# Optimization experiments

Measured on AMD Instinct MI355X. Metric: run time of the kernel, lower is better.

The kernel has to match this reference:

```python
import jax, jax.numpy as jnp
import numpy as np
import math

B, L, D, H = 2, 2048, 1024, 16
DK = D // H  # 64


def _lin(k, din, dout):
    kw, kb = jax.random.split(k)
    w = jax.random.normal(kw, (din, dout), dtype=jnp.float32) * 0.02
    b = jax.random.normal(kb, (dout,), dtype=jnp.float32) * 0.02
    return w, b


def setup_inputs() -> dict:
    key = jax.random.key(0)
    ks = jax.random.split(key, 12)
    wq, bq = _lin(ks[0], D, D)
    wk, bk = _lin(ks[1], D, D)
    wv, bv = _lin(ks[2], D, D)
    wo, bo = _lin(ks[3], D, D)
    whq, bhq = _lin(ks[4], DK, DK)
    whk, bhk = _lin(ks[5], DK, DK)
    whv, bhv = _lin(ks[6], DK, DK)
    who, bho = _lin(ks[7], DK, DK)
    return {
        "q_input": jax.random.normal(ks[8], (B, L, D), dtype=jnp.float32),
        "k_input": jax.random.normal(ks[9], (B, L, D), dtype=jnp.float32),
        "v_input": jax.random.normal(ks[10], (B, L, D), dtype=jnp.float32),
        "mask": jnp.ones((B, 1, L, L), dtype=jnp.int32),
        "wq": wq, "bq": bq, "wk": wk, "bk": bk, "wv": wv, "bv": bv,
        "wo": wo, "bo": bo,
        "whq": whq, "bhq": bhq, "whk": whk, "bhk": bhk,
        "whv": whv, "bhv": bhv, "who": who, "bho": bho,
    }


def reference(q_input, k_input, v_input, mask, wq, bq, wk, bk, wv, bv, wo, bo,
              whq, bhq, whk, bhk, whv, bhv, who, bho):
    scale = 1.0 / math.sqrt(DK)
    # Q/K/V projections -> [B, H, L, DK]
    Q = (q_input @ wq + bq).reshape(B, L, H, DK).transpose(0, 2, 1, 3)
    K = (k_input @ wk + bk).reshape(B, L, H, DK).transpose(0, 2, 1, 3)
    V = (v_input @ wv + bv).reshape(B, L, H, DK).transpose(0, 2, 1, 3)
    scores = jnp.einsum('bhqd,bhkd->bhqk', Q, K) * scale  # [B,H,L,L]
    neg = jnp.finfo(scores.dtype).min
    scores = jnp.where(mask == 0, neg, scores)
    probs = jax.nn.softmax(scores, axis=-1)  # dropout is identity in eval
    attn = jnp.einsum('bhqk,bhkd->bhqd', probs, V)
    heads = attn.transpose(0, 2, 1, 3)  # [B, L, H, DK]
    # Inter-head attention over the head dimension (size H) per position
    Qh = heads @ whq + bhq
    Kh = heads @ whk + bhk
    Vh = heads @ whv + bhv
    inter = jnp.einsum('blhd,blgd->blhg', Qh, Kh) * scale  # [B,L,H,H]
    iprobs = jax.nn.softmax(inter, axis=-1)
    mixed = jnp.einsum('blhg,blgd->blhd', iprobs, Vh)  # [B,L,H,DK]
    # note: inter_head_out is defined but unused in the original forward
    concat = mixed.reshape(B, L, D)
    return concat @ wo + bo
```

## Files before the change

kernel.cpp:

```cpp
#include <hip/hip_runtime.h>
#include <hip/hip_bf16.h>

typedef __bf16 bf16_t;
typedef __bf16 bf16x8 __attribute__((ext_vector_type(8)));
typedef float f32x4 __attribute__((ext_vector_type(4)));

__global__ void transpose_qkvw_kernel(const float* __restrict__ wq, const float* __restrict__ wk,
                                      const float* __restrict__ wv, bf16_t* __restrict__ wqkvT)
{
    __shared__ bf16_t tile[64][65];
    int z = blockIdx.z;
    const float* src = (z == 0) ? wq : (z == 1) ? wk : wv;
    bf16_t* dst = wqkvT + (size_t)z * 1048576;
    int rB = blockIdx.y * 64, cB = blockIdx.x * 64;
    int t = threadIdx.x;
#pragma unroll
    for (int i = 0; i < 16; i++) {
        int e = t + i * 256; int r = e >> 6, c = e & 63;
        tile[r][c] = (bf16_t)src[(size_t)(rB + r) * 1024 + cB + c];
    }
    __syncthreads();
#pragma unroll
    for (int i = 0; i < 16; i++) {
        int e = t + i * 256; int r = e >> 6, c = e & 63;
        dst[(size_t)(cB + r) * 1024 + rB + c] = tile[c][r];
    }
}

__global__ void transpose_one_kernel(const float* __restrict__ src, bf16_t* __restrict__ dst)
{
    __shared__ bf16_t tile[64][65];
    int rB = blockIdx.y * 64, cB = blockIdx.x * 64;
    int t = threadIdx.x;
#pragma unroll
    for (int i = 0; i < 16; i++) {
        int e = t + i * 256; int r = e >> 6, c = e & 63;
        tile[r][c] = (bf16_t)src[(size_t)(rB + r) * 1024 + cB + c];
    }
    __syncthreads();
#pragma unroll
    for (int i = 0; i < 16; i++) {
        int e = t + i * 256; int r = e >> 6, c = e & 63;
        dst[(size_t)(cB + r) * 1024 + rB + c] = tile[c][r];
    }
}

__global__ void transpose_small_kernel(const float* __restrict__ s0, const float* __restrict__ s1,
                                       const float* __restrict__ s2,
                                       bf16_t* __restrict__ d0, bf16_t* __restrict__ d1, bf16_t* __restrict__ d2)
{
    int z = blockIdx.x;
    const float* src = (z == 0) ? s0 : (z == 1) ? s1 : s2;
    bf16_t* dst = (z == 0) ? d0 : (z == 1) ? d1 : d2;
    int t = threadIdx.x;
#pragma unroll
    for (int i = 0; i < 16; i++) {
        int e = t + i * 256; int r = e >> 6, c = e & 63;
        dst[c * 64 + r] = (bf16_t)src[r * 64 + c];
    }
}

__global__ void maskflags_kernel(const int* __restrict__ mask, int* __restrict__ flags)
{
    int tile = blockIdx.x;
    int b = tile >> 10, qt = (tile >> 5) & 31, kt = tile & 31;
    int ok = 1;
#pragma unroll
    for (int i = 0; i < 16; i++) {
        int e = threadIdx.x + i * 256; int r = e >> 6, c = e & 63;
        ok &= (mask[((size_t)b * 2048 + qt * 64 + r) * 2048 + kt * 64 + c] != 0) ? 1 : 0;
    }
    ok = __syncthreads_and(ok);
    if (threadIdx.x == 0) flags[tile] = ok;
}

#define GS 40

__global__ __launch_bounds__(256, 2) void gemm_qkv_kernel(
    const float* __restrict__ Aq, const float* __restrict__ Ak, const float* __restrict__ Av,
    const bf16_t* __restrict__ WT,
    const float* __restrict__ bq, const float* __restrict__ bk, const float* __restrict__ bv,
    bf16_t* __restrict__ outbase)
{
    __shared__ bf16_t As[128 * GS];
    __shared__ bf16_t Bs[128 * GS];
    const int z = blockIdx.z;
    const float* A    = (z == 0) ? Aq : (z == 1) ? Ak : Av;
    const bf16_t* Bt  = WT + (size_t)z * 1048576;
    const float* bia  = (z == 0) ? bq : (z == 1) ? bk : bv;
    bf16_t* out = outbase + (size_t)z * 4194304;

    const int t = threadIdx.x;
    const int w = t >> 6, lane = t & 63;
    const int lane15 = lane & 15, quad = lane >> 4;
    const int wr = w >> 1, wc = w & 1;
    const int rowBase = blockIdx.y * 128, colBase = blockIdx.x * 128;

    const int ar = t >> 1, ac = (t & 1) * 16;
    const int e0 = t * 8, e1 = (256 + t) * 8;
    const int r0 = e0 >> 5, c0 = e0 & 31;
    const int r1 = e1 >> 5, c1 = e1 & 31;

    f32x4 acc[4][4];
    f32x4 zf = {0.f, 0.f, 0.f, 0.f};
#pragma unroll
    for (int i = 0; i < 4; i++)
#pragma unroll
        for (int j = 0; j < 4; j++) acc[i][j] = zf;

    for (int k0 = 0; k0 < 1024; k0 += 32) {
        const float4* ap = (const float4*)(A + (size_t)(rowBase + ar) * 1024 + k0 + ac);
        float4 af4[4];
#pragma unroll
        for (int i = 0; i < 4; i++) af4[i] = ap[i];
        bf16x8 b0 = *(const bf16x8*)(Bt + (size_t)(colBase + r0) * 1024 + k0 + c0);
        bf16x8 b1 = *(const bf16x8*)(Bt + (size_t)(colBase + r1) * 1024 + k0 + c1);
        bf16x8 av0, av1;
#pragma unroll
        for (int i = 0; i < 4; i++) {
            bf16x8& dstv = (i < 2) ? av0 : av1;
            int base = (i & 1) * 4;
            dstv[base + 0] = (bf16_t)af4[i].x; dstv[base + 1] = (bf16_t)af4[i].y;
            dstv[base + 2] = (bf16_t)af4[i].z; dstv[base + 3] = (bf16_t)af4[i].w;
        }
        *(bf16x8*)(As + ar * GS + ac) = av0;
        *(bf16x8*)(As + ar * GS + ac + 8) = av1;
        *(bf16x8*)(Bs + r0 * GS + c0) = b0;
        *(bf16x8*)(Bs + r1 * GS + c1) = b1;
        __syncthreads();
        bf16x8 afr[4], bfr[4];
#pragma unroll
        for (int mi = 0; mi < 4; mi++)
            afr[mi] = *(const bf16x8*)(As + (wr * 64 + mi * 16 + lane15) * GS + quad * 8);
#pragma unroll
        for (int ni = 0; ni < 4; ni++)
            bfr[ni] = *(const bf16x8*)(Bs + (wc * 64 + ni * 16 + lane15) * GS + quad * 8);
#pragma unroll
        for (int mi = 0; mi < 4; mi++)
#pragma unroll
            for (int ni = 0; ni < 4; ni++)
                acc[mi][ni] = __builtin_amdgcn_mfma_f32_16x16x32_bf16(afr[mi], bfr[ni], acc[mi][ni], 0, 0, 0);
        __syncthreads();
    }

#pragma unroll
    for (int ni = 0; ni < 4; ni++) {
        int col = colBase + wc * 64 + ni * 16 + lane15;
        float bias = bia[col];
        int h = col >> 6, dk = col & 63;
#pragma unroll
        for (int mi = 0; mi < 4; mi++) {
#pragma unroll
            for (int r = 0; r < 4; r++) {
                int row = rowBase + wr * 64 + mi * 16 + quad * 4 + r;
                int b = row >> 11, l = row & 2047;
                float v = acc[mi][ni][r] + bias;
                size_t dst = (z < 2) ? ((((size_t)(b * 16 + h)) * 2048 + l) * 64 + dk)
                                     : ((((size_t)(b * 16 + h)) * 64 + dk) * 2048 + l);
                out[dst] = (bf16_t)v;
            }
        }
    }
}

__global__ __launch_bounds__(256, 2) void gemm_out_kernel(
    const bf16_t* __restrict__ A, const bf16_t* __restrict__ Bt,
    const float* __restrict__ bia, float* __restrict__ out)
{
    __shared__ bf16_t As[128 * GS];
    __shared__ bf16_t Bs[128 * GS];
    const int t = threadIdx.x;
    const int w = t >> 6, lane = t & 63;
    const int lane15 = lane & 15, quad = lane >> 4;
    const int wr = w >> 1, wc = w & 1;
    const int rowBase = blockIdx.y * 128, colBase = blockIdx.x * 128;
    const int e0 = t * 8, e1 = (256 + t) * 8;
    const int r0 = e0 >> 5, c0 = e0 & 31;
    const int r1 = e1 >> 5, c1 = e1 & 31;

    f32x4 acc[4][4];
    f32x4 zf = {0.f, 0.f, 0.f, 0.f};
#pragma unroll
    for (int i = 0; i < 4; i++)
#pragma unroll
        for (int j = 0; j < 4; j++) acc[i][j] = zf;

    for (int k0 = 0; k0 < 1024; k0 += 32) {
        bf16x8 a0 = *(const bf16x8*)(A  + (size_t)(rowBase + r0) * 1024 + k0 + c0);
        bf16x8 a1 = *(const bf16x8*)(A  + (size_t)(rowBase + r1) * 1024 + k0 + c1);
        bf16x8 b0 = *(const bf16x8*)(Bt + (size_t)(colBase + r0) * 1024 + k0 + c0);
        bf16x8 b1 = *(const bf16x8*)(Bt + (size_t)(colBase + r1) * 1024 + k0 + c1);
        *(bf16x8*)(As + r0 * GS + c0) = a0;
        *(bf16x8*)(As + r1 * GS + c1) = a1;
        *(bf16x8*)(Bs + r0 * GS + c0) = b0;
        *(bf16x8*)(Bs + r1 * GS + c1) = b1;
        __syncthreads();
        bf16x8 afr[4], bfr[4];
#pragma unroll
        for (int mi = 0; mi < 4; mi++)
            afr[mi] = *(const bf16x8*)(As + (wr * 64 + mi * 16 + lane15) * GS + quad * 8);
#pragma unroll
        for (int ni = 0; ni < 4; ni++)
            bfr[ni] = *(const bf16x8*)(Bs + (wc * 64 + ni * 16 + lane15) * GS + quad * 8);
#pragma unroll
        for (int mi = 0; mi < 4; mi++)
#pragma unroll
            for (int ni = 0; ni < 4; ni++)
                acc[mi][ni] = __builtin_amdgcn_mfma_f32_16x16x32_bf16(afr[mi], bfr[ni], acc[mi][ni], 0, 0, 0);
        __syncthreads();
    }

#pragma unroll
    for (int ni = 0; ni < 4; ni++) {
        int col = colBase + wc * 64 + ni * 16 + lane15;
        float bias = bia[col];
#pragma unroll
        for (int mi = 0; mi < 4; mi++) {
#pragma unroll
            for (int r = 0; r < 4; r++) {
                int row = rowBase + wr * 64 + mi * 16 + quad * 4 + r;
                out[(size_t)row * 1024 + col] = acc[mi][ni][r] + bias;
            }
        }
    }
}

#define FS 72

__global__ __launch_bounds__(256, 2) void flash_kernel(
    const bf16_t* __restrict__ QKV, const int* __restrict__ mask,
    const int* __restrict__ flags, bf16_t* __restrict__ attnout)
{
    __shared__ bf16_t Ks[2][64 * FS];
    __shared__ bf16_t Vs[2][64 * FS];
    __shared__ bf16_t Ps[4 * 16 * FS];
    const int t = threadIdx.x, w = t >> 6, lane = t & 63;
    const int lane15 = lane & 15, quad = lane >> 4;
    const int qt = blockIdx.x, bh = blockIdx.y;
    const int b = bh >> 4, h = bh & 15;
    const bf16_t* Q  = QKV;
    const bf16_t* K  = QKV + 4194304;
    const bf16_t* Vt = QKV + 8388608;
    const int qrow0 = qt * 64 + w * 16;

    const bf16_t* qb = Q + ((size_t)bh * 2048 + qrow0 + lane15) * 64;
    bf16x8 aq0 = *(const bf16x8*)(qb + quad * 8);
    bf16x8 aq1 = *(const bf16x8*)(qb + 32 + quad * 8);
#pragma unroll
    for (int j = 0; j < 8; j++) {
        aq0[j] = (bf16_t)((float)aq0[j] * 0.125f);
        aq1[j] = (bf16_t)((float)aq1[j] * 0.125f);
    }

    f32x4 o[4];
    f32x4 zf = {0.f, 0.f, 0.f, 0.f};
#pragma unroll
    for (int df = 0; df < 4; df++) o[df] = zf;
    f32x4 lsum = zf;
    bf16_t* Pw = Ps + w * 16 * FS;
    bf16x8 ones;
#pragma unroll
    for (int j = 0; j < 8; j++) ones[j] = (bf16_t)1.0f;

    const int e0 = t * 8, e1 = (256 + t) * 8;
    const int kr0 = e0 >> 6, kc0 = e0 & 63, kr1 = e1 >> 6, kc1 = e1 & 63;
    const int* flagrow = flags + (b * 32 + qt) * 32;
    const bf16_t* Kb  = K  + (size_t)bh * 2048 * 64;
    const bf16_t* Vtb = Vt + (size_t)bh * 64 * 2048;

    {
        bf16x8 k0v = *(const bf16x8*)(Kb  + (size_t)kr0 * 64 + kc0);
        bf16x8 k1v = *(const bf16x8*)(Kb  + (size_t)kr1 * 64 + kc1);
        bf16x8 v0v = *(const bf16x8*)(Vtb + (size_t)kr0 * 2048 + kc0);
        bf16x8 v1v = *(const bf16x8*)(Vtb + (size_t)kr1 * 2048 + kc1);
        *(bf16x8*)(Ks[0] + kr0 * FS + kc0) = k0v;
        *(bf16x8*)(Ks[0] + kr1 * FS + kc1) = k1v;
        *(bf16x8*)(Vs[0] + kr0 * FS + kc0) = v0v;
        *(bf16x8*)(Vs[0] + kr1 * FS + kc1) = v1v;
    }
    __syncthreads();

    for (int kt = 0; kt < 32; kt++) {
        const int cur = kt & 1, nxt = cur ^ 1;
        bf16x8 k0v, k1v, v0v, v1v;
        if (kt + 1 < 32) {
            int kn = (kt + 1) * 64;
            k0v = *(const bf16x8*)(Kb  + (size_t)(kn + kr0) * 64 + kc0);
            k1v = *(const bf16x8*)(Kb  + (size_t)(kn + kr1) * 64 + kc1);
            v0v = *(const bf16x8*)(Vtb + (size_t)kr0 * 2048 + kn + kc0);
            v1v = *(const bf16x8*)(Vtb + (size_t)kr1 * 2048 + kn + kc1);
        }

        f32x4 sf[4];
#pragma unroll
        for (int nf = 0; nf < 4; nf++) {
            f32x4 a = zf;
            bf16x8 kb0 = *(const bf16x8*)(Ks[cur] + (nf * 16 + lane15) * FS + quad * 8);
            bf16x8 kb1 = *(const bf16x8*)(Ks[cur] + (nf * 16 + lane15) * FS + 32 + quad * 8);
            a = __builtin_amdgcn_mfma_f32_16x16x32_bf16(aq0, kb0, a, 0, 0, 0);
            a = __builtin_amdgcn_mfma_f32_16x16x32_bf16(aq1, kb1, a, 0, 0, 0);
            sf[nf] = a * 1.44269504f;
        }
        if (kt + 1 < 32) {
            *(bf16x8*)(Ks[nxt] + kr0 * FS + kc0) = k0v;
            *(bf16x8*)(Ks[nxt] + kr1 * FS + kc1) = k1v;
            *(bf16x8*)(Vs[nxt] + kr0 * FS + kc0) = v0v;
            *(bf16x8*)(Vs[nxt] + kr1 * FS + kc1) = v1v;
        }
        if (!flagrow[kt]) {
#pragma unroll
            for (int nf = 0; nf < 4; nf++)
#pragma unroll
                for (int r = 0; r < 4; r++) {
                    int qrow = qrow0 + quad * 4 + r;
                    int kpos = kt * 64 + nf * 16 + lane15;
                    if (mask[((size_t)b * 2048 + qrow) * 2048 + kpos] == 0)
                        sf[nf][r] = -1e30f;
                }
        }
#pragma unroll
        for (int nf = 0; nf < 4; nf++)
#pragma unroll
            for (int r = 0; r < 4; r++)
                Pw[(quad * 4 + r) * FS + nf * 16 + lane15] =
                    (bf16_t)exp2f(fminf(sf[nf][r], 80.f));

        bf16x8 pa0 = *(const bf16x8*)(Pw + lane15 * FS + quad * 8);
        bf16x8 pa1 = *(const bf16x8*)(Pw + lane15 * FS + 32 + quad * 8);
        lsum = __builtin_amdgcn_mfma_f32_16x16x32_bf16(pa0, ones, lsum, 0, 0, 0);
        lsum = __builtin_amdgcn_mfma_f32_16x16x32_bf16(pa1, ones, lsum, 0, 0, 0);
#pragma unroll
        for (int df = 0; df < 4; df++) {
            bf16x8 vb0 = *(const bf16x8*)(Vs[cur] + (df * 16 + lane15) * FS + quad * 8);
            bf16x8 vb1 = *(const bf16x8*)(Vs[cur] + (df * 16 + lane15) * FS + 32 + quad * 8);
            o[df] = __builtin_amdgcn_mfma_f32_16x16x32_bf16(pa0, vb0, o[df], 0, 0, 0);
            o[df] = __builtin_amdgcn_mfma_f32_16x16x32_bf16(pa1, vb1, o[df], 0, 0, 0);
        }
        __syncthreads();
    }
#pragma unroll
    for (int r = 0; r < 4; r++) {
        float inv = 1.0f / lsum[r];
        size_t row = (size_t)b * 2048 + qrow0 + quad * 4 + r;
#pragma unroll
        for (int df = 0; df < 4; df++)
            attnout[(row * 16 + h) * 64 + df * 16 + lane15] = (bf16_t)(o[df][r] * inv);
    }
}

__global__ __launch_bounds__(256, 2) void interhead_kernel(
    const bf16_t* __restrict__ attn,
    const bf16_t* __restrict__ whqT, const float* __restrict__ bhq,
    const bf16_t* __restrict__ whkT, const float* __restrict__ bhk,
    const bf16_t* __restrict__ whvT, const float* __restrict__ bhv,
    bf16_t* __restrict__ concat)
{
    __shared__ bf16_t lds[4 * 4608];
    const int t = threadIdx.x, w = t >> 6, lane = t & 63;
    const int lane15 = lane & 15, quad = lane >> 4;
    bf16_t* Qh  = lds + w * 4608;
    bf16_t* Kh  = Qh + 1024;
    bf16_t* VhT = Kh + 1024;
    bf16_t* P16 = VhT + 2048;
    const int p = blockIdx.x * 4 + w;

    bf16x8 z8 = {(bf16_t)0.f, (bf16_t)0.f, (bf16_t)0.f, (bf16_t)0.f,
                 (bf16_t)0.f, (bf16_t)0.f, (bf16_t)0.f, (bf16_t)0.f};
    ((bf16x8*)P16)[lane] = z8;
#pragma unroll
    for (int i = 0; i < 4; i++) ((bf16x8*)VhT)[i * 64 + lane] = z8;

    const bf16_t* hb = attn + ((size_t)p * 16 + lane15) * 64;
    bf16x8 ha0 = *(const bf16x8*)(hb + quad * 8);
    bf16x8 ha1 = *(const bf16x8*)(hb + 32 + quad * 8);

    const bf16_t* Wt[3] = {whqT, whkT, whvT};
    const float*  Bb[3] = {bhq, bhk, bhv};
    f32x4 zf = {0.f, 0.f, 0.f, 0.f};
#pragma unroll
    for (int m3 = 0; m3 < 3; m3++) {
#pragma unroll
        for (int nf = 0; nf < 4; nf++) {
            f32x4 acc = zf;
            bf16x8 wb0 = *(const bf16x8*)(Wt[m3] + (nf * 16 + lane15) * 64 + quad * 8);
            bf16x8 wb1 = *(const bf16x8*)(Wt[m3] + (nf * 16 + lane15) * 64 + 32 + quad * 8);
            acc = __builtin_amdgcn_mfma_f32_16x16x32_bf16(ha0, wb0, acc, 0, 0, 0);
            acc = __builtin_amdgcn_mfma_f32_16x16x32_bf16(ha1, wb1, acc, 0, 0, 0);
            float bias = Bb[m3][nf * 16 + lane15];
#pragma unroll
            for (int r = 0; r < 4; r++) {
                float v = acc[r] + bias;
                if (m3 == 0) v *= 0.125f;
                if (m3 == 2) VhT[(nf * 16 + lane15) * 32 + quad * 4 + r] = (bf16_t)v;
                else if (m3 == 0) Qh[(quad * 4 + r) * 64 + nf * 16 + lane15] = (bf16_t)v;
                else Kh[(quad * 4 + r) * 64 + nf * 16 + lane15] = (bf16_t)v;
            }
        }
    }
    __syncthreads();

    bf16x8 qa0 = *(const bf16x8*)(Qh + lane15 * 64 + quad * 8);
    bf16x8 qa1 = *(const bf16x8*)(Qh + lane15 * 64 + 32 + quad * 8);
    bf16x8 kb0 = *(const bf16x8*)(Kh + lane15 * 64 + quad * 8);
    bf16x8 kb1 = *(const bf16x8*)(Kh + lane15 * 64 + 32 + quad * 8);
    f32x4 s = zf;
    s = __builtin_amdgcn_mfma_f32_16x16x32_bf16(qa0, kb0, s, 0, 0, 0);
    s = __builtin_amdgcn_mfma_f32_16x16x32_bf16(qa1, kb1, s, 0, 0, 0);
#pragma unroll
    for (int r = 0; r < 4; r++) {
        float v = s[r];
        float mx = v;
        mx = fmaxf(mx, __shfl_xor(mx, 1));
        mx = fmaxf(mx, __shfl_xor(mx, 2));
        mx = fmaxf(mx, __shfl_xor(mx, 4));
        mx = fmaxf(mx, __shfl_xor(mx, 8));
        float pv = __expf(v - mx);
        float sm = pv;
        sm += __shfl_xor(sm, 1);
        sm += __shfl_xor(sm, 2);
        sm += __shfl_xor(sm, 4);
        sm += __shfl_xor(sm, 8);
        P16[(quad * 4 + r) * 32 + lane15] = (bf16_t)(pv / sm);
    }
    __syncthreads();

    bf16x8 pa = *(const bf16x8*)(P16 + lane15 * 32 + quad * 8);
    bf16_t* outp = concat + (size_t)p * 1024;
#pragma unroll
    for (int df = 0; df < 4; df++) {
        bf16x8 vb = *(const bf16x8*)(VhT + (df * 16 + lane15) * 32 + quad * 8);
        f32x4 mix = zf;
        mix = __builtin_amdgcn_mfma_f32_16x16x32_bf16(pa, vb, mix, 0, 0, 0);
#pragma unroll
        for (int r = 0; r < 4; r++)
            outp[(quad * 4 + r) * 64 + df * 16 + lane15] = (bf16_t)mix[r];
    }
}

extern "C" void kernel_launch(void* const* d_in, const int* in_sizes, int n_in,
                              void* d_out, int out_size, void* d_ws, size_t ws_size,
                              hipStream_t stream)
{
    const float* q_in = (const float*)d_in[0];
    const float* k_in = (const float*)d_in[1];
    const float* v_in = (const float*)d_in[2];
    const int*   mask = (const int*)d_in[3];
    const float* wq = (const float*)d_in[4];
    const float* bq = (const float*)d_in[5];
    const float* wk = (const float*)d_in[6];
    const float* bk = (const float*)d_in[7];
    const float* wv = (const float*)d_in[8];
    const float* bv = (const float*)d_in[9];
    const float* wo = (const float*)d_in[10];
    const float* bo = (const float*)d_in[11];
    const float* whq = (const float*)d_in[12];
    const float* bhq = (const float*)d_in[13];
    const float* whk = (const float*)d_in[14];
    const float* bhk = (const float*)d_in[15];
    const float* whv = (const float*)d_in[16];
    const float* bhv = (const float*)d_in[17];
    float* out = (float*)d_out;

    char* ws = (char*)d_ws;
    bf16_t* qkvb  = (bf16_t*)ws;
    bf16_t* concat = qkvb;
    bf16_t* woT   = (bf16_t*)(ws + 8u * 1024 * 1024);
    bf16_t* whqT  = (bf16_t*)(ws + 10u * 1024 * 1024);
    bf16_t* whkT  = whqT + 4096;
    bf16_t* whvT  = whqT + 8192;
    bf16_t* attnb = (bf16_t*)d_out;
    bf16_t* wqkvT = (bf16_t*)((char*)d_out + 8u * 1024 * 1024);
    int*    flags = (int*)((char*)d_out + 14u * 1024 * 1024);

    maskflags_kernel<<<2048, 256, 0, stream>>>(mask, flags);
    transpose_qkvw_kernel<<<dim3(16, 16, 3), 256, 0, stream>>>(wq, wk, wv, wqkvT);
    gemm_qkv_kernel<<<dim3(8, 32, 3), 256, 0, stream>>>(q_in, k_in, v_in, wqkvT, bq, bk, bv, qkvb);
    flash_kernel<<<dim3(32, 32), 256, 0, stream>>>(qkvb, mask, flags, attnb);
    transpose_one_kernel<<<dim3(16, 16), 256, 0, stream>>>(wo, woT);
    transpose_small_kernel<<<3, 256, 0, stream>>>(whq, whk, whv, whqT, whkT, whvT);
    interhead_kernel<<<1024, 256, 0, stream>>>(attnb, whqT, bhq, whkT, bhk, whvT, bhv, concat);
    gemm_out_kernel<<<dim3(8, 32), 256, 0, stream>>>(concat, woT, bo, out);
    (void)in_sizes; (void)n_in; (void)out_size; (void)ws_size;
}
```

Measured before the change: 352.3 us.

## Load K/V fragments directly from global memory in flash kernel, drop LDS staging

The flash attention kernel no longer stages K and V tiles through double-buffered shared memory. Each wave now reads its MFMA B-operand fragments straight from global memory, relying on L1/L2 cache for reuse across the four waves. This removes the per-iteration barrier and LDS traffic, and the launch bound is raised to 4 blocks per CU for occupancy. The exp2 input clamp is also dropped. The cost is redundant global loads per wave and no explicit prefetch overlap, plus a risk of overflow without the clamp (no max subtraction is done).

```diff
diff --git a/kernel.cpp b/kernel.cpp
--- a/kernel.cpp
+++ b/kernel.cpp
@@ -227,12 +227,10 @@
 
 #define FS 72
 
-__global__ __launch_bounds__(256, 2) void flash_kernel(
+__global__ __launch_bounds__(256, 4) void flash_kernel(
     const bf16_t* __restrict__ QKV, const int* __restrict__ mask,
     const int* __restrict__ flags, bf16_t* __restrict__ attnout)
 {
-    __shared__ bf16_t Ks[2][64 * FS];
-    __shared__ bf16_t Vs[2][64 * FS];
     __shared__ bf16_t Ps[4 * 16 * FS];
     const int t = threadIdx.x, w = t >> 6, lane = t & 63;
     const int lane15 = lane & 15, quad = lane >> 4;
@@ -262,50 +260,23 @@
 #pragma unroll
     for (int j = 0; j < 8; j++) ones[j] = (bf16_t)1.0f;
 
-    const int e0 = t * 8, e1 = (256 + t) * 8;
-    const int kr0 = e0 >> 6, kc0 = e0 & 63, kr1 = e1 >> 6, kc1 = e1 & 63;
     const int* flagrow = flags + (b * 32 + qt) * 32;
-    const bf16_t* Kb  = K  + (size_t)bh * 2048 * 64;
-    const bf16_t* Vtb = Vt + (size_t)bh * 64 * 2048;
-
-    {
-        bf16x8 k0v = *(const bf16x8*)(Kb  + (size_t)kr0 * 64 + kc0);
-        bf16x8 k1v = *(const bf16x8*)(Kb  + (size_t)kr1 * 64 + kc1);
-        bf16x8 v0v = *(const bf16x8*)(Vtb + (size_t)kr0 * 2048 + kc0);
-        bf16x8 v1v = *(const bf16x8*)(Vtb + (size_t)kr1 * 2048 + kc1);
-        *(bf16x8*)(Ks[0] + kr0 * FS + kc0) = k0v;
-        *(bf16x8*)(Ks[0] + kr1 * FS + kc1) = k1v;
-        *(bf16x8*)(Vs[0] + kr0 * FS + kc0) = v0v;
-        *(bf16x8*)(Vs[0] + kr1 * FS + kc1) = v1v;
-    }
-    __syncthreads();
+    const bf16_t* Kp = K  + (size_t)bh * 131072 + (size_t)lane15 * 64 + quad * 8;
+    const bf16_t* Vp = Vt + (size_t)bh * 131072 + (size_t)lane15 * 2048 + quad * 8;
 
     for (int kt = 0; kt < 32; kt++) {
-        const int cur = kt & 1, nxt = cur ^ 1;
-        bf16x8 k0v, k1v, v0v, v1v;
-        if (kt + 1 < 32) {
-            int kn = (kt + 1) * 64;
-            k0v = *(const bf16x8*)(Kb  + (size_t)(kn + kr0) * 64 + kc0);
-            k1v = *(const bf16x8*)(Kb  + (size_t)(kn + kr1) * 64 + kc1);
-            v0v = *(const bf16x8*)(Vtb + (size_t)kr0 * 2048 + kn + kc0);
-            v1v = *(const bf16x8*)(Vtb + (size_t)kr1 * 2048 + kn + kc1);
-        }
-
+        const bf16_t* Kt = Kp + (size_t)kt * 4096;
+        const bf16_t* Vk = Vp + kt * 64;
         f32x4 sf[4];
 #pragma unroll
         for (int nf = 0; nf < 4; nf++) {
+            const bf16_t* kr = Kt + nf * 1024;
+            bf16x8 kb0 = *(const bf16x8*)(kr);
+            bf16x8 kb1 = *(const bf16x8*)(kr + 32);
             f32x4 a = zf;
-            bf16x8 kb0 = *(const bf16x8*)(Ks[cur] + (nf * 16 + lane15) * FS + quad * 8);
-            bf16x8 kb1 = *(const bf16x8*)(Ks[cur] + (nf * 16 + lane15) * FS + 32 + quad * 8);
             a = __builtin_amdgcn_mfma_f32_16x16x32_bf16(aq0, kb0, a, 0, 0, 0);
             a = __builtin_amdgcn_mfma_f32_16x16x32_bf16(aq1, kb1, a, 0, 0, 0);
             sf[nf] = a * 1.44269504f;
-        }
-        if (kt + 1 < 32) {
-            *(bf16x8*)(Ks[nxt] + kr0 * FS + kc0) = k0v;
-            *(bf16x8*)(Ks[nxt] + kr1 * FS + kc1) = k1v;
-            *(bf16x8*)(Vs[nxt] + kr0 * FS + kc0) = v0v;
-            *(bf16x8*)(Vs[nxt] + kr1 * FS + kc1) = v1v;
         }
         if (!flagrow[kt]) {
 #pragma unroll
@@ -322,8 +293,7 @@
         for (int nf = 0; nf < 4; nf++)
 #pragma unroll
             for (int r = 0; r < 4; r++)
-                Pw[(quad * 4 + r) * FS + nf * 16 + lane15] =
-                    (bf16_t)exp2f(fminf(sf[nf][r], 80.f));
+                Pw[(quad * 4 + r) * FS + nf * 16 + lane15] = (bf16_t)exp2f(sf[nf][r]);
 
         bf16x8 pa0 = *(const bf16x8*)(Pw + lane15 * FS + quad * 8);
         bf16x8 pa1 = *(const bf16x8*)(Pw + lane15 * FS + 32 + quad * 8);
@@ -331,12 +301,12 @@
         lsum = __builtin_amdgcn_mfma_f32_16x16x32_bf16(pa1, ones, lsum, 0, 0, 0);
 #pragma unroll
         for (int df = 0; df < 4; df++) {
-            bf16x8 vb0 = *(const bf16x8*)(Vs[cur] + (df * 16 + lane15) * FS + quad * 8);
-            bf16x8 vb1 = *(const bf16x8*)(Vs[cur] + (df * 16 + lane15) * FS + 32 + quad * 8);
+            const bf16_t* vr = Vk + (size_t)df * 32768;
+            bf16x8 vb0 = *(const bf16x8*)(vr);
+            bf16x8 vb1 = *(const bf16x8*)(vr + 32);
             o[df] = __builtin_amdgcn_mfma_f32_16x16x32_bf16(pa0, vb0, o[df], 0, 0, 0);
             o[df] = __builtin_amdgcn_mfma_f32_16x16x32_bf16(pa1, vb1, o[df], 0, 0, 0);
         }
-        __syncthreads();
     }
 #pragma unroll
     for (int r = 0; r < 4; r++) {
```

Result: slower. 489.8 us (+39.0%).
